# Kernel optimization log

Measured on AMD Instinct MI355X. Metric: run time of the kernel, lower is better.

## Reference

```python
import jax, jax.numpy as jnp
import numpy as np


def setup_inputs() -> dict:
    key = jax.random.key(0)
    ks = jax.random.split(key, 8)
    B, De, Do, T, H, W = 4, 128, 512, 4, 30, 52
    s = 0.05  # weight init scale
    return {
        "m_in": jax.random.normal(ks[0], (B, De, T, H, W), jnp.float32),
        "m_out": jax.random.normal(ks[1], (B, Do, T, H, W), jnp.float32),
        "q_in": jax.random.normal(ks[2], (B, De, H, W), jnp.float32),
        "q_out": jax.random.normal(ks[3], (B, Do, H, W), jnp.float32),
        "wr": jax.random.normal(ks[4], (Do, 2 * Do), jnp.float32) * s,
        "br": jnp.zeros((Do,), jnp.float32),
        "wu": jax.random.normal(ks[5], (Do, 2 * Do), jnp.float32) * s,
        "bu": jnp.zeros((Do,), jnp.float32),
        "wc": jax.random.normal(ks[6], (Do, 2 * Do), jnp.float32) * s,
        "bc": jnp.zeros((Do,), jnp.float32),
    }


def reference(m_in, m_out, q_in, q_out, wr, br, wu, bu, wc, bc):
    B, De, T, H, W = m_in.shape
    Do = m_out.shape[1]
    PROP_LAYERS = 5

    # --- memory read: pairwise frame attention (bmm + softmax + bmm) ---
    # keys: all T memory frames flattened; queries: current frame.
    mi = m_in.reshape(B, De, T * H * W)            # [B, De, THW]
    qi = q_in.reshape(B, De, H * W)                # [B, De, HW]
    p = jnp.einsum('bdk,bdq->bkq', mi, qi) / (De ** 0.5)  # [B, THW, HW]
    p = jax.nn.softmax(p, axis=1)                  # softmax over memory locations (dim=1 in torch)
    mem = jnp.einsum('bok,bkq->boq', m_out.reshape(B, Do, T * H * W), p)
    mem = mem.reshape(B, Do, H, W)                 # mem_mean; identical every propagate layer

    # --- ConvGRU_h (kernel_size=1 => per-pixel linear gates) ---
    def conv1x1(w, b, x):
        return jnp.einsum('oc,bchw->bohw', w, x) + b[None, :, None, None]

    def gru(x, h):
        xh = jnp.concatenate([x, h], axis=1)                       # [B, 2*Do, H, W]
        r = jax.nn.sigmoid(conv1x1(wr, br, xh))
        u = jax.nn.sigmoid(conv1x1(wu, bu, xh))
        c = jnp.tanh(conv1x1(wc, bc, jnp.concatenate([x, r * h], axis=1)))
        return h * (1.0 - u) + u * c

    q0 = q_out
    q = q_out
    for _ in range(PROP_LAYERS):
        q = gru(q, mem)  # original: q_out = ConvGRU_h(q_out, mem_mean)
    return jnp.concatenate([q, q0], axis=1)  # [B, 2*Do, H, W]
```

## Files before the change

kernel.cpp:

```cpp
#include <hip/hip_runtime.h>
#include <hip/hip_bf16.h>
#include <math.h>

typedef unsigned short u16;
typedef __attribute__((ext_vector_type(8))) short bf16x8;
typedef __attribute__((ext_vector_type(4))) float f32x4;

__device__ __forceinline__ u16 f2bf(float f) {
  union { float f; unsigned u; } x; x.f = f;
  unsigned r = x.u + 0x7fffu + ((x.u >> 16) & 1u);
  return (u16)(r >> 16);
}
__device__ __forceinline__ float bf2f(u16 h) {
  union { unsigned u; float f; } x; x.u = ((unsigned)h) << 16;
  return x.f;
}
__device__ __forceinline__ float sigmf(float x) {
  x = fminf(fmaxf(x, -30.f), 30.f);
  return 1.f / (1.f + __expf(-x));
}
__device__ __forceinline__ float tanh_fast(float x) {
  x = fminf(fmaxf(x, -15.f), 15.f);
  float t = __expf(2.f * x);
  return (t - 1.f) / (t + 1.f);
}

#define NB 4
#define DE 128
#define DO_ 512
#define HW 1560
#define THW 6240
#define NP 1664
#define KP 6272
#define PROP 5

template<int MODE, int BMT, int BKT>
__global__ __launch_bounds__(256)
void gemm_bt(const u16* __restrict__ A, const u16* __restrict__ Bt,
             int K, int lda, int ldb, long a_bs, long b_bs,
             void* __restrict__ out0v, long o0_bs, int ld0,
             u16* __restrict__ out1, long o1_bs, int ld1,
             const void* __restrict__ e0v, long e0_bs,
             const void* __restrict__ e1v, long e1_bs,
             const void* __restrict__ e2v, long e2_bs,
             int nvalid, float scale)
{
  constexpr int WR = BMT / 64;
  constexpr int WC = 4 / WR;
  constexpr int NF = 8 / WC;
  constexpr int KK = BKT / 32;
  constexpr int ASLOT = BMT * BKT / 8;
  constexpr int BSLOT = 128 * BKT / 8;
  constexpr int NISS = (ASLOT + BSLOT) / 256;
  constexpr int RSH = (BMT == 128) ? 7 : 6;
  __shared__ u16 lds[2][ASLOT + BSLOT][8];

  const int tid = threadIdx.x;
  const int wave = tid >> 6, lane = tid & 63;
  const int kg = lane >> 4, lr = lane & 15;
  const int wrw = wave / WC, wcw = wave % WC;
  const long b = blockIdx.z;
  const int m0 = blockIdx.x * BMT, n0 = blockIdx.y * 128;
  A += b * a_bs; Bt += b * b_bs;

  float* out0f = (float*)out0v;
  u16* out0h = (u16*)out0v;
  const float* e0f = (const float*)e0v;
  const u16* e0h = (const u16*)e0v;
  const u16* e1h = (const u16*)e1v;
  const u16* e2h = (const u16*)e2v;

  auto stage = [&](int buf, int kt) {
#pragma unroll
    for (int i = 0; i < NISS; ++i) {
      int s = tid + 256 * i;
      const u16* src;
      if (s < ASLOT) {
        int row = s & (BMT - 1), g = s >> RSH;
        src = A + (long)(m0 + row) * lda + kt + g * 8;
      } else {
        int s2 = s - ASLOT;
        int row = s2 & 127, g = s2 >> 7;
        src = Bt + (long)(n0 + row) * ldb + kt + g * 8;
      }
      __builtin_amdgcn_global_load_lds(
          (const __attribute__((address_space(1))) void*)src,
          (__attribute__((address_space(3))) void*)&lds[buf][wave * 64 + 256 * i][0],
          16, 0, 0);
    }
  };

  f32x4 acc[4][NF];
#pragma unroll
  for (int m = 0; m < 4; ++m)
#pragma unroll
    for (int n = 0; n < NF; ++n) acc[m][n] = (f32x4){0.f, 0.f, 0.f, 0.f};

  const int nt = K / BKT;
  stage(0, 0);
  __syncthreads();
  for (int t = 0; t < nt; ++t) {
    int cur = t & 1;
    if (t + 1 < nt) stage(cur ^ 1, (t + 1) * BKT);
    bf16x8 af[KK][4], bfr[KK][NF];
#pragma unroll
    for (int kk = 0; kk < KK; ++kk) {
#pragma unroll
      for (int m = 0; m < 4; ++m)
        af[kk][m] = *(const bf16x8*)&lds[cur][(kk * 4 + kg) * BMT + wrw * 64 + m * 16 + lr][0];
#pragma unroll
      for (int n = 0; n < NF; ++n)
        bfr[kk][n] = *(const bf16x8*)&lds[cur][ASLOT + (kk * 4 + kg) * 128 + (wcw * NF + n) * 16 + lr][0];
    }
#pragma unroll
    for (int kk = 0; kk < KK; ++kk)
#pragma unroll
      for (int m = 0; m < 4; ++m)
#pragma unroll
        for (int n = 0; n < NF; ++n)
          acc[m][n] = __builtin_amdgcn_mfma_f32_16x16x32_bf16(af[kk][m], bfr[kk][n], acc[m][n], 0, 0, 0);
    __syncthreads();
  }

  if constexpr (MODE == 0) {
    float rs[4][4];
#pragma unroll
    for (int m = 0; m < 4; ++m)
#pragma unroll
      for (int j = 0; j < 4; ++j) rs[m][j] = 0.f;
#pragma unroll
    for (int m = 0; m < 4; ++m) {
      int rloc = wrw * 64 + m * 16 + kg * 4;
#pragma unroll
      for (int n = 0; n < NF; ++n) {
        int col = n0 + (wcw * NF + n) * 16 + lr;
#pragma unroll
        for (int j = 0; j < 4; ++j) {
          long row = m0 + rloc + j;
          float p = __expf(acc[m][n][j] * scale);
          bool valid = (col < nvalid);
          out1[b * o1_bs + row * ld1 + col] = valid ? f2bf(p) : (u16)0;
          rs[m][j] += valid ? p : 0.f;
        }
      }
    }
#pragma unroll
    for (int m = 0; m < 4; ++m)
#pragma unroll
      for (int j = 0; j < 4; ++j) {
#pragma unroll
        for (int msk = 1; msk < 16; msk <<= 1)
          rs[m][j] += __shfl_xor(rs[m][j], msk, 64);
      }
    float* zbuf = (float*)lds;
    if (lr == 0) {
#pragma unroll
      for (int m = 0; m < 4; ++m)
#pragma unroll
        for (int j = 0; j < 4; ++j)
          zbuf[wcw * 128 + wrw * 64 + m * 16 + kg * 4 + j] = rs[m][j];
    }
    __syncthreads();
    if (tid < 128)
      out0f[b * o0_bs + (long)blockIdx.y * NP + (m0 + tid)] = zbuf[tid] + zbuf[128 + tid];
    return;
  }

#pragma unroll
  for (int m = 0; m < 4; ++m) {
    int rloc = wrw * 64 + m * 16 + kg * 4;
#pragma unroll
    for (int n = 0; n < NF; ++n) {
      int col = n0 + (wcw * NF + n) * 16 + lr;
#pragma unroll
      for (int j = 0; j < 4; ++j) {
        long row = m0 + rloc + j;
        float v = acc[m][n][j];
        if constexpr (MODE == 2) {
          out1[b * o1_bs + row * ld1 + col] = f2bf(v + e0f[col]);
        } else if constexpr (MODE == 3) {
          float gt = sigmf(v + bf2f(e0h[b * e0_bs + row * 1024 + col]));
          if (col < 512)
            out1[b * o1_bs + row * ld1 + 512 + col] =
                f2bf(gt * bf2f(e1h[b * e1_bs + row * 512 + col]));
          else
            out0h[b * o0_bs + row * ld0 + (col - 512)] = f2bf(gt);
        } else if constexpr (MODE == 4) {
          float cg = tanh_fast(v + e0f[col]);
          float u = bf2f(e1h[b * e1_bs + row * 512 + col]);
          float mm = bf2f(e2h[b * e2_bs + row * 512 + col]);
          float x = mm * (1.f - u) + u * cg;
          out1[b * o1_bs + row * ld1 + col] = f2bf(x);
          if (out0f) out0f[b * o0_bs + row * ld0 + col] = x;
        }
      }
    }
  }
}

__global__ __launch_bounds__(256, 2)
void gemm_pv(const u16* __restrict__ Pt, const u16* __restrict__ moutb,
             u16* __restrict__ Ppart)
{
  const int bid = blockIdx.x;
  const int xcd = bid & 7, j = bid >> 3;
  const int bz = 2 * xcd + (j >= 26);
  const int mb = (j >= 26) ? (j - 26) : j;
  const int b = bz >> 2, z = bz & 3;
  const int m0 = mb * 64;
  const int k0 = z * 1568;

  const u16* A = Pt + (long)b * NP * KP;
  const u16* B0;
  {
    const u16* Bb = moutb + (long)b * DO_ * KP;
    B0 = Bb + (long)((threadIdx.x >> 6) * 128 + (threadIdx.x & 15)) * KP + ((threadIdx.x & 63) >> 4) * 8;
  }

  __shared__ u16 lds[2][2048];
  const int tid = threadIdx.x;
  const int wave = tid >> 6, lane = tid & 63;
  const int kg = lane >> 4, lr = lane & 15;

  auto stage = [&](int buf, int kt) {
    int row = tid & 63, g = tid >> 6;
    const u16* src = A + (long)(m0 + row) * KP + kt + g * 8;
    __builtin_amdgcn_global_load_lds(
        (const __attribute__((address_space(1))) void*)src,
        (__attribute__((address_space(3))) void*)&lds[buf][(wave * 64) * 8],
        16, 0, 0);
  };

  f32x4 acc[4][8];
#pragma unroll
  for (int m = 0; m < 4; ++m)
#pragma unroll
    for (int n = 0; n < 8; ++n) acc[m][n] = (f32x4){0.f, 0.f, 0.f, 0.f};

  bf16x8 bra[8], brb[8];
#pragma unroll
  for (int n = 0; n < 8; ++n)
    bra[n] = *(const bf16x8*)&B0[(long)n * 16 * KP + k0];
  stage(0, k0);
  __syncthreads();

#define PV_STEP(BU, BL, T, CUR)                                                  \
  {                                                                              \
    if ((T) + 1 < 49) {                                                          \
      int ktn = k0 + ((T) + 1) * 32;                                             \
      _Pragma("unroll") for (int n = 0; n < 8; ++n)                              \
          BL[n] = *(const bf16x8*)&B0[(long)n * 16 * KP + ktn];                  \
      stage((CUR) ^ 1, ktn);                                                     \
    }                                                                            \
    bf16x8 af[4];                                                                \
    _Pragma("unroll") for (int m = 0; m < 4; ++m)                                \
        af[m] = *(const bf16x8*)&lds[CUR][(kg * 64 + m * 16 + lr) * 8];          \
    _Pragma("unroll") for (int m = 0; m < 4; ++m)                                \
        _Pragma("unroll") for (int n = 0; n < 8; ++n)                            \
            acc[m][n] = __builtin_amdgcn_mfma_f32_16x16x32_bf16(af[m], BU[n],    \
                                                                acc[m][n], 0, 0, 0); \
    __syncthreads();                                                             \
  }

  for (int tp = 0; tp < 24; ++tp) {
    PV_STEP(bra, brb, 2 * tp, 0);
    PV_STEP(brb, bra, 2 * tp + 1, 1);
  }
  PV_STEP(bra, brb, 48, 0);
#undef PV_STEP

  u16* out = Ppart + (long)bz * NP * DO_;
#pragma unroll
  for (int m = 0; m < 4; ++m) {
#pragma unroll
    for (int n = 0; n < 8; ++n) {
      int col = wave * 128 + n * 16 + lr;
#pragma unroll
      for (int j = 0; j < 4; ++j) {
        int row = m0 + m * 16 + kg * 4 + j;
        out[(long)row * DO_ + col] = f2bf(acc[m][n][j]);
      }
    }
  }
}

__global__ void k_transpose_cast(const float* __restrict__ in, u16* __restrict__ out,
                                 int R, int C, int Cp, int out_ld,
                                 long in_bs, long out_bs) {
  __shared__ float t[32][33];
  long b = blockIdx.z;
  int c0 = blockIdx.x * 32, r0 = blockIdx.y * 32;
  int tx = threadIdx.x, ty = threadIdx.y;
#pragma unroll
  for (int i = 0; i < 32; i += 8) {
    int r = r0 + ty + i, c = c0 + tx;
    t[ty + i][tx] = (r < R && c < C) ? in[b * in_bs + (long)r * C + c] : 0.f;
  }
  __syncthreads();
#pragma unroll
  for (int i = 0; i < 32; i += 8) {
    int c = c0 + ty + i, r = r0 + tx;
    if (c < Cp && r < R)
      out[b * out_bs + (long)c * out_ld + r] = f2bf(t[tx][ty + i]);
  }
}

__global__ void k_cast_pad(const float* __restrict__ in, u16* __restrict__ out,
                           int Cin, int Cout, long in_bs, long out_bs) {
  int c = blockIdx.x * 256 + threadIdx.x;
  int r = blockIdx.y;
  long b = blockIdx.z;
  if (c >= Cout) return;
  out[b * out_bs + (long)r * Cout + c] =
      (c < Cin) ? f2bf(in[b * in_bs + (long)r * Cin + c]) : (u16)0;
}

__global__ void k_build_wru(const float* __restrict__ wr_, const float* __restrict__ wu_,
                            u16* __restrict__ wrux, u16* __restrict__ wruh) {
  int k = blockIdx.x * 256 + threadIdx.x;
  int m = blockIdx.y;
  if (k >= 512) return;
  const float* src = (m < 512) ? wr_ : wu_;
  int mm = m & 511;
  wrux[m * 512 + k] = f2bf(src[mm * 1024 + k]);
  wruh[m * 512 + k] = f2bf(src[mm * 1024 + 512 + k]);
}

__global__ void k_bias_ru(const float* __restrict__ br_, const float* __restrict__ bu_,
                          float* __restrict__ bias) {
  int i = blockIdx.x * 256 + threadIdx.x;
  if (i < 1024) bias[i] = (i < 512) ? br_[i] : bu_[i - 512];
}

__global__ void k_invz(const float* __restrict__ Zp, float* __restrict__ invZ) {
  int t = blockIdx.x * 256 + threadIdx.x;
  if (t >= NB * NP) return;
  int b = t / NP, q = t - b * NP;
  const float* base = Zp + (long)b * 49 * NP + q;
  float s = 0.f;
#pragma unroll
  for (int nb = 0; nb < 49; ++nb) s += base[(long)nb * NP];
  invZ[t] = 1.f / s;
}

__global__ void k_reduce_mem(const u16* __restrict__ Ppart, const float* __restrict__ invZ,
                             u16* __restrict__ memTb) {
  long t = (long)blockIdx.x * 256 + threadIdx.x;
  const long bs = (long)NP * DO_;
  if (t >= (long)NB * bs / 8) return;
  long flat = t * 8;
  int b = (int)(flat / bs);
  long r = flat - (long)b * bs;
  int q = (int)(r / DO_);
  float s[8];
#pragma unroll
  for (int e = 0; e < 8; ++e) s[e] = 0.f;
#pragma unroll
  for (int z = 0; z < 4; ++z) {
    uint4 v = *(const uint4*)&Ppart[(long)(b * 4 + z) * bs + r];
    s[0] += bf2f((u16)(v.x & 0xffff)); s[1] += bf2f((u16)(v.x >> 16));
    s[2] += bf2f((u16)(v.y & 0xffff)); s[3] += bf2f((u16)(v.y >> 16));
    s[4] += bf2f((u16)(v.z & 0xffff)); s[5] += bf2f((u16)(v.z >> 16));
    s[6] += bf2f((u16)(v.w & 0xffff)); s[7] += bf2f((u16)(v.w >> 16));
  }
  float iz = invZ[b * NP + q];
  uint4 o;
  o.x = (unsigned)f2bf(s[0] * iz) | ((unsigned)f2bf(s[1] * iz) << 16);
  o.y = (unsigned)f2bf(s[2] * iz) | ((unsigned)f2bf(s[3] * iz) << 16);
  o.z = (unsigned)f2bf(s[4] * iz) | ((unsigned)f2bf(s[5] * iz) << 16);
  o.w = (unsigned)f2bf(s[6] * iz) | ((unsigned)f2bf(s[7] * iz) << 16);
  *(uint4*)&memTb[(long)b * bs + r] = o;
}

__global__ void k_out_q(const float* __restrict__ Qfin, float* __restrict__ dout) {
  __shared__ float t[32][33];
  long b = blockIdx.z;
  int q0 = blockIdx.x * 32, ch0 = blockIdx.y * 32;
  int tx = threadIdx.x, ty = threadIdx.y;
#pragma unroll
  for (int i = 0; i < 32; i += 8)
    t[ty + i][tx] = Qfin[b * ((long)NP * 512) + (long)(q0 + ty + i) * 512 + ch0 + tx];
  __syncthreads();
#pragma unroll
  for (int i = 0; i < 32; i += 8) {
    int ch = ch0 + ty + i, q = q0 + tx;
    if (q < HW)
      dout[b * ((long)1024 * HW) + (long)ch * HW + q] = t[tx][ty + i];
  }
}

__global__ void k_copy_q0(const float4* __restrict__ src, float4* __restrict__ dst) {
  int idx = blockIdx.x * 256 + threadIdx.x;
  long b = blockIdx.z;
  const long n4 = (long)DO_ * HW / 4;
  if (idx < n4)
    dst[b * ((long)1024 * HW / 4) + n4 + idx] = src[b * n4 + idx];
}

extern "C" void kernel_launch(void* const* d_in, const int* in_sizes, int n_in,
                              void* d_out, int out_size, void* d_ws, size_t ws_size,
                              hipStream_t stream) {
  const float* m_in  = (const float*)d_in[0];
  const float* m_out = (const float*)d_in[1];
  const float* q_in  = (const float*)d_in[2];
  const float* q_out = (const float*)d_in[3];
  const float* wr    = (const float*)d_in[4];
  const float* br    = (const float*)d_in[5];
  const float* wu    = (const float*)d_in[6];
  const float* bu    = (const float*)d_in[7];
  const float* wc    = (const float*)d_in[8];
  const float* bc    = (const float*)d_in[9];
  float* dout = (float*)d_out;

  char* p = (char*)d_ws;
  size_t off = 0;
  auto alloc = [&](size_t bytes) { void* r = p + off; off += (bytes + 255) & ~(size_t)255; return r; };
  u16*   miT    = (u16*)alloc((size_t)NB * KP * DE * 2);
  u16*   qiT    = (u16*)alloc((size_t)NB * NP * DE * 2);
  u16*   Pt     = (u16*)alloc((size_t)NB * NP * KP * 2);
  float* invZ   = (float*)alloc((size_t)NB * NP * 4);
  u16*   moutb  = (u16*)alloc((size_t)NB * DO_ * KP * 2);
  u16*   memTb  = (u16*)alloc((size_t)NB * NP * DO_ * 2);
  u16*   chru   = (u16*)alloc((size_t)NB * NP * 1024 * 2);
  u16*   U      = (u16*)alloc((size_t)NB * NP * DO_ * 2);
  u16*   XRb    = (u16*)alloc((size_t)NB * NP * 1024 * 2);
  u16*   XRa    = (u16*)alloc((size_t)NB * NP * 1024 * 2);
  float* Qfin   = (float*)alloc((size_t)NB * NP * DO_ * 4);
  u16*   wrux   = (u16*)alloc((size_t)1024 * 512 * 2);
  u16*   wruh   = (u16*)alloc((size_t)1024 * 512 * 2);
  u16*   wcb    = (u16*)alloc((size_t)512 * 1024 * 2);
  float* biasru = (float*)alloc((size_t)1024 * 4);
  u16*   Ppart  = (u16*)chru;
  float* Zp     = (float*)memTb;
  if (off > ws_size) return;

  k_build_wru<<<dim3(2, 1024), 256, 0, stream>>>(wr, wu, wrux, wruh);
  k_cast_pad<<<dim3(4, 512, 1), 256, 0, stream>>>(wc, wcb, 1024, 1024, 0, 0);
  k_bias_ru<<<dim3(4), 256, 0, stream>>>(br, bu, biasru);
  k_cast_pad<<<dim3(25, 512, NB), 256, 0, stream>>>(
      m_out, moutb, THW, KP, (long)DO_ * THW, (long)DO_ * KP);
  k_transpose_cast<<<dim3(196, 4, NB), dim3(32, 8), 0, stream>>>(
      m_in, miT, DE, THW, KP, DE, (long)DE * THW, (long)KP * DE);
  k_transpose_cast<<<dim3(52, 4, NB), dim3(32, 8), 0, stream>>>(
      q_in, qiT, DE, HW, NP, DE, (long)DE * HW, (long)NP * DE);
  k_transpose_cast<<<dim3(52, 16, NB), dim3(32, 8), 0, stream>>>(
      q_out, XRa, DO_, HW, NP, 1024, (long)DO_ * HW, (long)NP * 1024);

  gemm_bt<0, 128, 32><<<dim3(13, 49, NB), 256, 0, stream>>>(
      qiT, miT, DE, DE, DE, (long)NP * DE, (long)KP * DE,
      Zp, (long)49 * NP, 0, Pt, (long)NP * KP, KP,
      nullptr, 0, nullptr, 0, nullptr, 0, THW, 0.08838834764831845f);
  k_invz<<<dim3(26), 256, 0, stream>>>(Zp, invZ);

  gemm_pv<<<dim3(416), 256, 0, stream>>>(Pt, moutb, Ppart);
  k_reduce_mem<<<dim3(1664), 256, 0, stream>>>(Ppart, invZ, memTb);

  gemm_bt<2, 64, 64><<<dim3(26, 8, NB), 256, 0, stream>>>(
      memTb, wruh, DO_, DO_, DO_, (long)NP * DO_, 0,
      nullptr, 0, 0, chru, (long)NP * 1024, 1024,
      biasru, 0, nullptr, 0, nullptr, 0, 0, 0.f);

  u16* xr[2] = {XRa, XRb};
  for (int l = 0; l < PROP; ++l) {
    u16* cur = xr[l & 1];
    u16* nxt = xr[(l + 1) & 1];
    gemm_bt<3, 64, 64><<<dim3(26, 8, NB), 256, 0, stream>>>(
        cur, wrux, DO_, 1024, DO_, (long)NP * 1024, 0,
        U, (long)NP * DO_, DO_, cur, (long)NP * 1024, 1024,
        chru, (long)NP * 1024, memTb, (long)NP * DO_, nullptr, 0, 0, 0.f);
    gemm_bt<4, 64, 64><<<dim3(26, 4, NB), 256, 0, stream>>>(
        cur, wcb, 1024, 1024, 1024, (long)NP * 1024, 0,
        (l == PROP - 1) ? (void*)Qfin : nullptr, (long)NP * DO_, DO_,
        nxt, (long)NP * 1024, 1024,
        bc, 0, U, (long)NP * DO_, memTb, (long)NP * DO_, 0, 0.f);
  }

  k_out_q<<<dim3(49, 16, NB), dim3(32, 8), 0, stream>>>(Qfin, dout);
  k_copy_q0<<<dim3(780, 1, NB), 256, 0, stream>>>((const float4*)q_out, (float4*)dout);
}
```

Baseline: 679.1 us.

## Stage A tile fully in LDS, stream B from global, split PV seven ways

Replaces the double-buffered LDS GEMM with a kernel that loads the whole A row-tile (full K) into LDS once, then reads B fragments straight from global memory. This drops the per-iteration K-loop barriers and B staging. The cost is larger LDS per block (up to 64KB for the wc GEMM) and reliance on cache for B reuse. The PV GEMM moves from a 4-way split-K with XCD-aware block mapping to a plain 7-way split-K grid, and the reduce kernel and workspace layout change to match the larger partial buffer.

```diff
diff --git a/kernel.cpp b/kernel.cpp
--- a/kernel.cpp
+++ b/kernel.cpp
@@ -33,11 +33,13 @@
 #define NP 1664
 #define KP 6272
 #define PROP 5
-
-template<int MODE, int BMT, int BKT>
+#define PVSPLIT 7
+#define PVKC 896
+
+template<int MODE, int ROWS, int KTOT>
 __global__ __launch_bounds__(256)
-void gemm_bt(const u16* __restrict__ A, const u16* __restrict__ Bt,
-             int K, int lda, int ldb, long a_bs, long b_bs,
+void gemm_ws(const u16* __restrict__ A, const u16* __restrict__ Bt,
+             int lda, int ldb, long a_bs, long b_bs,
              void* __restrict__ out0v, long o0_bs, int ld0,
              u16* __restrict__ out1, long o1_bs, int ld1,
              const void* __restrict__ e0v, long e0_bs,
@@ -45,22 +47,17 @@
              const void* __restrict__ e2v, long e2_bs,
              int nvalid, float scale)
 {
-  constexpr int WR = BMT / 64;
-  constexpr int WC = 4 / WR;
-  constexpr int NF = 8 / WC;
-  constexpr int KK = BKT / 32;
-  constexpr int ASLOT = BMT * BKT / 8;
-  constexpr int BSLOT = 128 * BKT / 8;
-  constexpr int NISS = (ASLOT + BSLOT) / 256;
-  constexpr int RSH = (BMT == 128) ? 7 : 6;
-  __shared__ u16 lds[2][ASLOT + BSLOT][8];
+  constexpr int MF = ROWS / 16;
+  constexpr int SLOTS = ROWS * KTOT / 8;
+  constexpr int NLD = SLOTS / 256;
+  constexpr int RSH = (ROWS == 64) ? 6 : 5;
+  __shared__ u16 lds[SLOTS][8];
 
   const int tid = threadIdx.x;
   const int wave = tid >> 6, lane = tid & 63;
   const int kg = lane >> 4, lr = lane & 15;
-  const int wrw = wave / WC, wcw = wave % WC;
   const long b = blockIdx.z;
-  const int m0 = blockIdx.x * BMT, n0 = blockIdx.y * 128;
+  const int m0 = blockIdx.x * ROWS, n0 = blockIdx.y * 128;
   A += b * a_bs; Bt += b * b_bs;
 
   float* out0f = (float*)out0v;
@@ -70,73 +67,57 @@
   const u16* e1h = (const u16*)e1v;
   const u16* e2h = (const u16*)e2v;
 
-  auto stage = [&](int buf, int kt) {
-#pragma unroll
-    for (int i = 0; i < NISS; ++i) {
-      int s = tid + 256 * i;
-      const u16* src;
-      if (s < ASLOT) {
-        int row = s & (BMT - 1), g = s >> RSH;
-        src = A + (long)(m0 + row) * lda + kt + g * 8;
-      } else {
-        int s2 = s - ASLOT;
-        int row = s2 & 127, g = s2 >> 7;
-        src = Bt + (long)(n0 + row) * ldb + kt + g * 8;
-      }
-      __builtin_amdgcn_global_load_lds(
-          (const __attribute__((address_space(1))) void*)src,
-          (__attribute__((address_space(3))) void*)&lds[buf][wave * 64 + 256 * i][0],
-          16, 0, 0);
-    }
-  };
-
-  f32x4 acc[4][NF];
-#pragma unroll
-  for (int m = 0; m < 4; ++m)
-#pragma unroll
-    for (int n = 0; n < NF; ++n) acc[m][n] = (f32x4){0.f, 0.f, 0.f, 0.f};
-
-  const int nt = K / BKT;
-  stage(0, 0);
+#pragma unroll
+  for (int i = 0; i < NLD; ++i) {
+    int s = tid + 256 * i;
+    int row = s & (ROWS - 1), g = s >> RSH;
+    const u16* src = A + (long)(m0 + row) * lda + g * 8;
+    __builtin_amdgcn_global_load_lds(
+        (const __attribute__((address_space(1))) void*)src,
+        (__attribute__((address_space(3))) void*)&lds[wave * 64 + 256 * i][0],
+        16, 0, 0);
+  }
   __syncthreads();
-  for (int t = 0; t < nt; ++t) {
-    int cur = t & 1;
-    if (t + 1 < nt) stage(cur ^ 1, (t + 1) * BKT);
-    bf16x8 af[KK][4], bfr[KK][NF];
-#pragma unroll
-    for (int kk = 0; kk < KK; ++kk) {
-#pragma unroll
-      for (int m = 0; m < 4; ++m)
-        af[kk][m] = *(const bf16x8*)&lds[cur][(kk * 4 + kg) * BMT + wrw * 64 + m * 16 + lr][0];
-#pragma unroll
-      for (int n = 0; n < NF; ++n)
-        bfr[kk][n] = *(const bf16x8*)&lds[cur][ASLOT + (kk * 4 + kg) * 128 + (wcw * NF + n) * 16 + lr][0];
-    }
-#pragma unroll
-    for (int kk = 0; kk < KK; ++kk)
-#pragma unroll
-      for (int m = 0; m < 4; ++m)
-#pragma unroll
-        for (int n = 0; n < NF; ++n)
-          acc[m][n] = __builtin_amdgcn_mfma_f32_16x16x32_bf16(af[kk][m], bfr[kk][n], acc[m][n], 0, 0, 0);
-    __syncthreads();
+
+  f32x4 acc[MF][2];
+#pragma unroll
+  for (int m = 0; m < MF; ++m)
+#pragma unroll
+    for (int n = 0; n < 2; ++n) acc[m][n] = (f32x4){0.f, 0.f, 0.f, 0.f};
+
+  const u16* Bp0 = Bt + (long)(n0 + wave * 32 + lr) * ldb + kg * 8;
+  const u16* Bp1 = Bp0 + 16 * ldb;
+
+  constexpr int NK = KTOT / 32;
+#pragma unroll 4
+  for (int g2 = 0; g2 < NK; ++g2) {
+    bf16x8 af[MF], bf[2];
+#pragma unroll
+    for (int m = 0; m < MF; ++m)
+      af[m] = *(const bf16x8*)&lds[(g2 * 4 + kg) * ROWS + m * 16 + lr][0];
+    bf[0] = *(const bf16x8*)&Bp0[g2 * 32];
+    bf[1] = *(const bf16x8*)&Bp1[g2 * 32];
+#pragma unroll
+    for (int m = 0; m < MF; ++m)
+#pragma unroll
+      for (int n = 0; n < 2; ++n)
+        acc[m][n] = __builtin_amdgcn_mfma_f32_16x16x32_bf16(af[m], bf[n], acc[m][n], 0, 0, 0);
   }
 
   if constexpr (MODE == 0) {
-    float rs[4][4];
-#pragma unroll
-    for (int m = 0; m < 4; ++m)
+    float rs[MF][4];
+#pragma unroll
+    for (int m = 0; m < MF; ++m)
 #pragma unroll
       for (int j = 0; j < 4; ++j) rs[m][j] = 0.f;
 #pragma unroll
-    for (int m = 0; m < 4; ++m) {
-      int rloc = wrw * 64 + m * 16 + kg * 4;
-#pragma unroll
-      for (int n = 0; n < NF; ++n) {
-        int col = n0 + (wcw * NF + n) * 16 + lr;
+    for (int m = 0; m < MF; ++m) {
+#pragma unroll
+      for (int n = 0; n < 2; ++n) {
+        int col = n0 + wave * 32 + n * 16 + lr;
 #pragma unroll
         for (int j = 0; j < 4; ++j) {
-          long row = m0 + rloc + j;
+          long row = m0 + m * 16 + kg * 4 + j;
           float p = __expf(acc[m][n][j] * scale);
           bool valid = (col < nvalid);
           out1[b * o1_bs + row * ld1 + col] = valid ? f2bf(p) : (u16)0;
@@ -145,36 +126,37 @@
       }
     }
 #pragma unroll
-    for (int m = 0; m < 4; ++m)
+    for (int m = 0; m < MF; ++m)
 #pragma unroll
       for (int j = 0; j < 4; ++j) {
 #pragma unroll
         for (int msk = 1; msk < 16; msk <<= 1)
           rs[m][j] += __shfl_xor(rs[m][j], msk, 64);
       }
-    float* zbuf = (float*)lds;
+    __syncthreads();
+    float* zbuf = (float*)&lds[0][0];
     if (lr == 0) {
 #pragma unroll
-      for (int m = 0; m < 4; ++m)
+      for (int m = 0; m < MF; ++m)
 #pragma unroll
         for (int j = 0; j < 4; ++j)
-          zbuf[wcw * 128 + wrw * 64 + m * 16 + kg * 4 + j] = rs[m][j];
+          zbuf[wave * 64 + m * 16 + kg * 4 + j] = rs[m][j];
     }
     __syncthreads();
-    if (tid < 128)
-      out0f[b * o0_bs + (long)blockIdx.y * NP + (m0 + tid)] = zbuf[tid] + zbuf[128 + tid];
+    if (tid < 64)
+      out0f[b * o0_bs + (long)blockIdx.y * NP + (m0 + tid)] =
+          zbuf[tid] + zbuf[64 + tid] + zbuf[128 + tid] + zbuf[192 + tid];
     return;
   }
 
 #pragma unroll
-  for (int m = 0; m < 4; ++m) {
-    int rloc = wrw * 64 + m * 16 + kg * 4;
-#pragma unroll
-    for (int n = 0; n < NF; ++n) {
-      int col = n0 + (wcw * NF + n) * 16 + lr;
+  for (int m = 0; m < MF; ++m) {
+#pragma unroll
+    for (int n = 0; n < 2; ++n) {
+      int col = n0 + wave * 32 + n * 16 + lr;
 #pragma unroll
       for (int j = 0; j < 4; ++j) {
-        long row = m0 + rloc + j;
+        long row = m0 + m * 16 + kg * 4 + j;
         float v = acc[m][n][j];
         if constexpr (MODE == 2) {
           out1[b * o1_bs + row * ld1 + col] = f2bf(v + e0f[col]);
@@ -202,19 +184,17 @@
 void gemm_pv(const u16* __restrict__ Pt, const u16* __restrict__ moutb,
              u16* __restrict__ Ppart)
 {
-  const int bid = blockIdx.x;
-  const int xcd = bid & 7, j = bid >> 3;
-  const int bz = 2 * xcd + (j >= 26);
-  const int mb = (j >= 26) ? (j - 26) : j;
-  const int b = bz >> 2, z = bz & 3;
-  const int m0 = mb * 64;
-  const int k0 = z * 1568;
+  const int m0 = blockIdx.x * 64;
+  const int z = blockIdx.y;
+  const int b = blockIdx.z;
+  const int k0 = z * PVKC;
 
   const u16* A = Pt + (long)b * NP * KP;
   const u16* B0;
   {
     const u16* Bb = moutb + (long)b * DO_ * KP;
-    B0 = Bb + (long)((threadIdx.x >> 6) * 128 + (threadIdx.x & 15)) * KP + ((threadIdx.x & 63) >> 4) * 8;
+    B0 = Bb + (long)((threadIdx.x >> 6) * 128 + (threadIdx.x & 15)) * KP +
+         ((threadIdx.x & 63) >> 4) * 8;
   }
 
   __shared__ u16 lds[2][2048];
@@ -246,7 +226,7 @@
 
 #define PV_STEP(BU, BL, T, CUR)                                                  \
   {                                                                              \
-    if ((T) + 1 < 49) {                                                          \
+    if ((T) + 1 < 28) {                                                          \
       int ktn = k0 + ((T) + 1) * 32;                                             \
       _Pragma("unroll") for (int n = 0; n < 8; ++n)                              \
           BL[n] = *(const bf16x8*)&B0[(long)n * 16 * KP + ktn];                  \
@@ -262,14 +242,13 @@
     __syncthreads();                                                             \
   }
 
-  for (int tp = 0; tp < 24; ++tp) {
+  for (int tp = 0; tp < 14; ++tp) {
     PV_STEP(bra, brb, 2 * tp, 0);
     PV_STEP(brb, bra, 2 * tp + 1, 1);
   }
-  PV_STEP(bra, brb, 48, 0);
 #undef PV_STEP
 
-  u16* out = Ppart + (long)bz * NP * DO_;
+  u16* out = Ppart + (long)(b * PVSPLIT + z) * NP * DO_;
 #pragma unroll
   for (int m = 0; m < 4; ++m) {
 #pragma unroll
@@ -356,8 +335,8 @@
 #pragma unroll
   for (int e = 0; e < 8; ++e) s[e] = 0.f;
 #pragma unroll
-  for (int z = 0; z < 4; ++z) {
-    uint4 v = *(const uint4*)&Ppart[(long)(b * 4 + z) * bs + r];
+  for (int z = 0; z < PVSPLIT; ++z) {
+    uint4 v = *(const uint4*)&Ppart[(long)(b * PVSPLIT + z) * bs + r];
     s[0] += bf2f((u16)(v.x & 0xffff)); s[1] += bf2f((u16)(v.x >> 16));
     s[2] += bf2f((u16)(v.y & 0xffff)); s[3] += bf2f((u16)(v.y >> 16));
     s[4] += bf2f((u16)(v.z & 0xffff)); s[5] += bf2f((u16)(v.z >> 16));
@@ -424,8 +403,8 @@
   u16*   chru   = (u16*)alloc((size_t)NB * NP * 1024 * 2);
   u16*   U      = (u16*)alloc((size_t)NB * NP * DO_ * 2);
   u16*   XRb    = (u16*)alloc((size_t)NB * NP * 1024 * 2);
+  float* Qfin   = (float*)alloc((size_t)NB * NP * DO_ * 4);
   u16*   XRa    = (u16*)alloc((size_t)NB * NP * 1024 * 2);
-  float* Qfin   = (float*)alloc((size_t)NB * NP * DO_ * 4);
   u16*   wrux   = (u16*)alloc((size_t)1024 * 512 * 2);
   u16*   wruh   = (u16*)alloc((size_t)1024 * 512 * 2);
   u16*   wcb    = (u16*)alloc((size_t)512 * 1024 * 2);
@@ -446,17 +425,17 @@
   k_transpose_cast<<<dim3(52, 16, NB), dim3(32, 8), 0, stream>>>(
       q_out, XRa, DO_, HW, NP, 1024, (long)DO_ * HW, (long)NP * 1024);
 
-  gemm_bt<0, 128, 32><<<dim3(13, 49, NB), 256, 0, stream>>>(
-      qiT, miT, DE, DE, DE, (long)NP * DE, (long)KP * DE,
+  gemm_ws<0, 64, 128><<<dim3(26, 49, NB), 256, 0, stream>>>(
+      qiT, miT, DE, DE, (long)NP * DE, (long)KP * DE,
       Zp, (long)49 * NP, 0, Pt, (long)NP * KP, KP,
       nullptr, 0, nullptr, 0, nullptr, 0, THW, 0.08838834764831845f);
   k_invz<<<dim3(26), 256, 0, stream>>>(Zp, invZ);
 
-  gemm_pv<<<dim3(416), 256, 0, stream>>>(Pt, moutb, Ppart);
+  gemm_pv<<<dim3(26, PVSPLIT, NB), 256, 0, stream>>>(Pt, moutb, Ppart);
   k_reduce_mem<<<dim3(1664), 256, 0, stream>>>(Ppart, invZ, memTb);
 
-  gemm_bt<2, 64, 64><<<dim3(26, 8, NB), 256, 0, stream>>>(
-      memTb, wruh, DO_, DO_, DO_, (long)NP * DO_, 0,
+  gemm_ws<2, 64, 512><<<dim3(26, 8, NB), 256, 0, stream>>>(
+      memTb, wruh, DO_, DO_, (long)NP * DO_, 0,
       nullptr, 0, 0, chru, (long)NP * 1024, 1024,
       biasru, 0, nullptr, 0, nullptr, 0, 0, 0.f);
 
@@ -464,12 +443,12 @@
   for (int l = 0; l < PROP; ++l) {
     u16* cur = xr[l & 1];
     u16* nxt = xr[(l + 1) & 1];
-    gemm_bt<3, 64, 64><<<dim3(26, 8, NB), 256, 0, stream>>>(
-        cur, wrux, DO_, 1024, DO_, (long)NP * 1024, 0,
+    gemm_ws<3, 64, 512><<<dim3(26, 8, NB), 256, 0, stream>>>(
+        cur, wrux, 1024, DO_, (long)NP * 1024, 0,
         U, (long)NP * DO_, DO_, cur, (long)NP * 1024, 1024,
         chru, (long)NP * 1024, memTb, (long)NP * DO_, nullptr, 0, 0, 0.f);
-    gemm_bt<4, 64, 64><<<dim3(26, 4, NB), 256, 0, stream>>>(
-        cur, wcb, 1024, 1024, 1024, (long)NP * 1024, 0,
+    gemm_ws<4, 32, 1024><<<dim3(52, 4, NB), 256, 0, stream>>>(
+        cur, wcb, 1024, 1024, (long)NP * 1024, 0,
         (l == PROP - 1) ? (void*)Qfin : nullptr, (long)NP * DO_, DO_,
         nxt, (long)NP * 1024, 1024,
         bc, 0, U, (long)NP * DO_, memTb, (long)NP * DO_, 0, 0.f);
```

Result: slower. 745.8 us (+9.8%).

## Use explicit vmcnt waits with split barriers and widen PV split-K to seven

Applied to the files above, without the earlier changes.

Replaces __syncthreads in the GEMM main loops with explicit s_waitcnt vmcnt counts plus raw s_barrier, so the next tile's global-to-LDS loads stay in flight during the current tile's MFMAs. The PV GEMM split-K factor rises from 4 to 7 (896-wide K chunks, 728 blocks with a new XCD-aware mapping) and its launch-bounds occupancy hint is dropped. This gives the device more parallelism and a shorter per-block loop, at the cost of more partial buffers for the reduction kernel to read. The hand-counted vmcnt values must match the issued loads or LDS reads become racy. The workspace order also changes so Qfin sits inside the Ppart aliased region.

```diff
diff --git a/kernel.cpp b/kernel.cpp
--- a/kernel.cpp
+++ b/kernel.cpp
@@ -23,6 +23,14 @@
   x = fminf(fmaxf(x, -15.f), 15.f);
   float t = __expf(2.f * x);
   return (t - 1.f) / (t + 1.f);
+}
+
+template<int N> __device__ __forceinline__ void wait_vmcnt() {
+  if constexpr (N == 0)      asm volatile("s_waitcnt vmcnt(0)" ::: "memory");
+  else if constexpr (N == 4) asm volatile("s_waitcnt vmcnt(4)" ::: "memory");
+  else if constexpr (N == 6) asm volatile("s_waitcnt vmcnt(6)" ::: "memory");
+  else if constexpr (N == 9) asm volatile("s_waitcnt vmcnt(9)" ::: "memory");
+  else static_assert(N == 0 || N == 4 || N == 6 || N == 9, "add vmcnt case");
 }
 
 #define NB 4
@@ -33,17 +41,19 @@
 #define NP 1664
 #define KP 6272
 #define PROP 5
+#define PVSPLIT 7
+#define PVKC 896
 
 template<int MODE, int BMT, int BKT>
-__global__ __launch_bounds__(256)
-void gemm_bt(const u16* __restrict__ A, const u16* __restrict__ Bt,
-             int K, int lda, int ldb, long a_bs, long b_bs,
-             void* __restrict__ out0v, long o0_bs, int ld0,
-             u16* __restrict__ out1, long o1_bs, int ld1,
-             const void* __restrict__ e0v, long e0_bs,
-             const void* __restrict__ e1v, long e1_bs,
-             const void* __restrict__ e2v, long e2_bs,
-             int nvalid, float scale)
+__device__ __forceinline__
+void gemm_core(const u16* __restrict__ A, const u16* __restrict__ Bt,
+               int K, int lda, int ldb, long a_bs, long b_bs,
+               void* __restrict__ out0v, long o0_bs, int ld0,
+               u16* __restrict__ out1, long o1_bs, int ld1,
+               const void* __restrict__ e0v, long e0_bs,
+               const void* __restrict__ e1v, long e1_bs,
+               const void* __restrict__ e2v, long e2_bs,
+               int nvalid, float scale)
 {
   constexpr int WR = BMT / 64;
   constexpr int WC = 4 / WR;
@@ -98,10 +108,15 @@
 
   const int nt = K / BKT;
   stage(0, 0);
-  __syncthreads();
   for (int t = 0; t < nt; ++t) {
     int cur = t & 1;
-    if (t + 1 < nt) stage(cur ^ 1, (t + 1) * BKT);
+    if (t + 1 < nt) {
+      stage(cur ^ 1, (t + 1) * BKT);
+      wait_vmcnt<NISS>();
+    } else {
+      wait_vmcnt<0>();
+    }
+    __builtin_amdgcn_s_barrier();
     bf16x8 af[KK][4], bfr[KK][NF];
 #pragma unroll
     for (int kk = 0; kk < KK; ++kk) {
@@ -119,7 +134,7 @@
 #pragma unroll
         for (int n = 0; n < NF; ++n)
           acc[m][n] = __builtin_amdgcn_mfma_f32_16x16x32_bf16(af[kk][m], bfr[kk][n], acc[m][n], 0, 0, 0);
-    __syncthreads();
+    __builtin_amdgcn_s_barrier();
   }
 
   if constexpr (MODE == 0) {
@@ -198,23 +213,38 @@
   }
 }
 
-__global__ __launch_bounds__(256, 2)
+#define GEMM_ARGS                                                              \
+  const u16* __restrict__ A, const u16* __restrict__ Bt, int K, int lda,       \
+  int ldb, long a_bs, long b_bs, void* __restrict__ out0v, long o0_bs,         \
+  int ld0, u16* __restrict__ out1, long o1_bs, int ld1,                        \
+  const void* __restrict__ e0v, long e0_bs, const void* __restrict__ e1v,      \
+  long e1_bs, const void* __restrict__ e2v, long e2_bs, int nvalid, float scale
+#define GEMM_PASS A, Bt, K, lda, ldb, a_bs, b_bs, out0v, o0_bs, ld0, out1,     \
+  o1_bs, ld1, e0v, e0_bs, e1v, e1_bs, e2v, e2_bs, nvalid, scale
+
+__global__ __launch_bounds__(256) void gk_scores(GEMM_ARGS) { gemm_core<0, 128, 32>(GEMM_PASS); }
+__global__ __launch_bounds__(256) void gk_chru(GEMM_ARGS)   { gemm_core<2, 64, 64>(GEMM_PASS); }
+__global__ __launch_bounds__(256) void gk_gates(GEMM_ARGS)  { gemm_core<3, 64, 64>(GEMM_PASS); }
+__global__ __launch_bounds__(256) void gk_cand(GEMM_ARGS)   { gemm_core<4, 64, 64>(GEMM_PASS); }
+
+__global__ __launch_bounds__(256)
 void gemm_pv(const u16* __restrict__ Pt, const u16* __restrict__ moutb,
              u16* __restrict__ Ppart)
 {
   const int bid = blockIdx.x;
-  const int xcd = bid & 7, j = bid >> 3;
-  const int bz = 2 * xcd + (j >= 26);
-  const int mb = (j >= 26) ? (j - 26) : j;
-  const int b = bz >> 2, z = bz & 3;
+  const int xcd = bid & 7, i = bid >> 3;
+  const int s = xcd * 91 + i;
+  const int pair = s / 26, mb = s - pair * 26;
+  const int b = pair / PVSPLIT, z = pair - b * PVSPLIT;
   const int m0 = mb * 64;
-  const int k0 = z * 1568;
+  const int k0 = z * PVKC;
 
   const u16* A = Pt + (long)b * NP * KP;
   const u16* B0;
   {
     const u16* Bb = moutb + (long)b * DO_ * KP;
-    B0 = Bb + (long)((threadIdx.x >> 6) * 128 + (threadIdx.x & 15)) * KP + ((threadIdx.x & 63) >> 4) * 8;
+    B0 = Bb + (long)((threadIdx.x >> 6) * 128 + (threadIdx.x & 15)) * KP +
+         ((threadIdx.x & 63) >> 4) * 8;
   }
 
   __shared__ u16 lds[2][2048];
@@ -242,16 +272,19 @@
   for (int n = 0; n < 8; ++n)
     bra[n] = *(const bf16x8*)&B0[(long)n * 16 * KP + k0];
   stage(0, k0);
-  __syncthreads();
 
 #define PV_STEP(BU, BL, T, CUR)                                                  \
   {                                                                              \
-    if ((T) + 1 < 49) {                                                          \
+    if ((T) + 1 < 28) {                                                          \
       int ktn = k0 + ((T) + 1) * 32;                                             \
       _Pragma("unroll") for (int n = 0; n < 8; ++n)                              \
           BL[n] = *(const bf16x8*)&B0[(long)n * 16 * KP + ktn];                  \
       stage((CUR) ^ 1, ktn);                                                     \
+      wait_vmcnt<9>();                                                           \
+    } else {                                                                     \
+      wait_vmcnt<0>();                                                           \
     }                                                                            \
+    __builtin_amdgcn_s_barrier();                                                \
     bf16x8 af[4];                                                                \
     _Pragma("unroll") for (int m = 0; m < 4; ++m)                                \
         af[m] = *(const bf16x8*)&lds[CUR][(kg * 64 + m * 16 + lr) * 8];          \
@@ -259,17 +292,16 @@
         _Pragma("unroll") for (int n = 0; n < 8; ++n)                            \
             acc[m][n] = __builtin_amdgcn_mfma_f32_16x16x32_bf16(af[m], BU[n],    \
                                                                 acc[m][n], 0, 0, 0); \
-    __syncthreads();                                                             \
-  }
-
-  for (int tp = 0; tp < 24; ++tp) {
+    __builtin_amdgcn_s_barrier();                                                \
+  }
+
+  for (int tp = 0; tp < 14; ++tp) {
     PV_STEP(bra, brb, 2 * tp, 0);
     PV_STEP(brb, bra, 2 * tp + 1, 1);
   }
-  PV_STEP(bra, brb, 48, 0);
 #undef PV_STEP
 
-  u16* out = Ppart + (long)bz * NP * DO_;
+  u16* out = Ppart + (long)(b * PVSPLIT + z) * NP * DO_;
 #pragma unroll
   for (int m = 0; m < 4; ++m) {
 #pragma unroll
@@ -356,8 +388,8 @@
 #pragma unroll
   for (int e = 0; e < 8; ++e) s[e] = 0.f;
 #pragma unroll
-  for (int z = 0; z < 4; ++z) {
-    uint4 v = *(const uint4*)&Ppart[(long)(b * 4 + z) * bs + r];
+  for (int z = 0; z < PVSPLIT; ++z) {
+    uint4 v = *(const uint4*)&Ppart[(long)(b * PVSPLIT + z) * bs + r];
     s[0] += bf2f((u16)(v.x & 0xffff)); s[1] += bf2f((u16)(v.x >> 16));
     s[2] += bf2f((u16)(v.y & 0xffff)); s[3] += bf2f((u16)(v.y >> 16));
     s[4] += bf2f((u16)(v.z & 0xffff)); s[5] += bf2f((u16)(v.z >> 16));
@@ -424,8 +456,8 @@
   u16*   chru   = (u16*)alloc((size_t)NB * NP * 1024 * 2);
   u16*   U      = (u16*)alloc((size_t)NB * NP * DO_ * 2);
   u16*   XRb    = (u16*)alloc((size_t)NB * NP * 1024 * 2);
+  float* Qfin   = (float*)alloc((size_t)NB * NP * DO_ * 4);
   u16*   XRa    = (u16*)alloc((size_t)NB * NP * 1024 * 2);
-  float* Qfin   = (float*)alloc((size_t)NB * NP * DO_ * 4);
   u16*   wrux   = (u16*)alloc((size_t)1024 * 512 * 2);
   u16*   wruh   = (u16*)alloc((size_t)1024 * 512 * 2);
   u16*   wcb    = (u16*)alloc((size_t)512 * 1024 * 2);
@@ -446,16 +478,16 @@
   k_transpose_cast<<<dim3(52, 16, NB), dim3(32, 8), 0, stream>>>(
       q_out, XRa, DO_, HW, NP, 1024, (long)DO_ * HW, (long)NP * 1024);
 
-  gemm_bt<0, 128, 32><<<dim3(13, 49, NB), 256, 0, stream>>>(
+  gk_scores<<<dim3(13, 49, NB), 256, 0, stream>>>(
       qiT, miT, DE, DE, DE, (long)NP * DE, (long)KP * DE,
       Zp, (long)49 * NP, 0, Pt, (long)NP * KP, KP,
       nullptr, 0, nullptr, 0, nullptr, 0, THW, 0.08838834764831845f);
   k_invz<<<dim3(26), 256, 0, stream>>>(Zp, invZ);
 
-  gemm_pv<<<dim3(416), 256, 0, stream>>>(Pt, moutb, Ppart);
+  gemm_pv<<<dim3(728), 256, 0, stream>>>(Pt, moutb, Ppart);
   k_reduce_mem<<<dim3(1664), 256, 0, stream>>>(Ppart, invZ, memTb);
 
-  gemm_bt<2, 64, 64><<<dim3(26, 8, NB), 256, 0, stream>>>(
+  gk_chru<<<dim3(26, 8, NB), 256, 0, stream>>>(
       memTb, wruh, DO_, DO_, DO_, (long)NP * DO_, 0,
       nullptr, 0, 0, chru, (long)NP * 1024, 1024,
       biasru, 0, nullptr, 0, nullptr, 0, 0, 0.f);
@@ -464,11 +496,11 @@
   for (int l = 0; l < PROP; ++l) {
     u16* cur = xr[l & 1];
     u16* nxt = xr[(l + 1) & 1];
-    gemm_bt<3, 64, 64><<<dim3(26, 8, NB), 256, 0, stream>>>(
+    gk_gates<<<dim3(26, 8, NB), 256, 0, stream>>>(
         cur, wrux, DO_, 1024, DO_, (long)NP * 1024, 0,
         U, (long)NP * DO_, DO_, cur, (long)NP * 1024, 1024,
         chru, (long)NP * 1024, memTb, (long)NP * DO_, nullptr, 0, 0, 0.f);
-    gemm_bt<4, 64, 64><<<dim3(26, 4, NB), 256, 0, stream>>>(
+    gk_cand<<<dim3(26, 4, NB), 256, 0, stream>>>(
         cur, wcb, 1024, 1024, 1024, (long)NP * 1024, 0,
         (l == PROP - 1) ? (void*)Qfin : nullptr, (long)NP * DO_, DO_,
         nxt, (long)NP * 1024, 1024,
```

Result: no change. 680.7 us (+0.2%).
